# Performance work log

Hardware: AMD Instinct MI355X
Metric: run time of the kernel (lower is better)

## Reference

```python
import jax, jax.numpy as jnp
import numpy as np

ARCH = (1024, 2048, 2048, 512)
STEPS = 20
LR = 0.1
BATCH = 4096


def setup_inputs() -> dict:
    key = jax.random.key(0)
    ks = jax.random.split(key, 1 + len(ARCH) - 1)
    x = jax.random.normal(ks[0], (BATCH, ARCH[0]), dtype=jnp.float32)
    inp = {"x": x}
    # forward layers: weight (out, in) as in torch nn.Linear, orthogonal-ish init gain sqrt(2)
    for i in range(len(ARCH) - 1):
        fan_in = ARCH[i]
        W = jax.random.normal(ks[1 + i], (ARCH[i + 1], fan_in), dtype=jnp.float32) * jnp.sqrt(2.0 / fan_in)
        inp[f"W{i}"] = W
        inp[f"b{i}"] = jnp.zeros((ARCH[i + 1],), dtype=jnp.float32)
    return inp


def _errors(r, Ws):
    # errors[-1] = r[-1]; errors[i] = r[i] - tanh(F.linear(r[i+1], W_i.T)) = r[i] - tanh(r[i+1] @ W_i)
    errs = [None] * len(ARCH)
    errs[-1] = r[-1]
    for i in range(len(Ws) - 1, -1, -1):
        errs[i] = r[i] - jnp.tanh(r[i + 1] @ Ws[i])  # (B, arch[i])
    return errs


def _pc_forward(x, Ws, bs):
    # initialize states with a no-grad feedforward pass (torch.no_grad -> stop_gradient)
    r = [x]
    t = x
    for W, b in zip(Ws, bs):
        t = jnp.tanh(t @ W.T + b)
        r.append(jax.lax.stop_gradient(t))

    def step(carry, _):
        r = list(carry)
        errs = _errors(r, Ws)
        new_r = [r[0]]  # r[0] = x, fixed
        for i in range(1, len(ARCH)):
            feedback = errs[i - 1] @ Ws[i - 1].T  # F.linear(errors[i-1], W)
            new_r.append(r[i] + LR * (-errs[i] + feedback))
        return tuple(new_r), None

    r, _ = jax.lax.scan(step, tuple(r), None, length=STEPS)
    r = list(r)
    final_errs = _errors(r, Ws)
    total_error = 0.5 * sum(jnp.sum(e * e) for e in final_errs)
    return r[-1], total_error


def reference(x, W0, b0, W1, b1, W2, b2):
    Ws = [W0, W1, W2]
    bs = [b0, b1, b2]
    return _pc_forward(x, Ws, bs)
```

## Files before the change

### kernel.cpp

```cpp
#include <hip/hip_runtime.h>

typedef unsigned short u16;
typedef __bf16 bf16_t;
typedef bf16_t bf16x8 __attribute__((ext_vector_type(8)));
typedef u16 u16x8 __attribute__((ext_vector_type(8)));
typedef float f32x4 __attribute__((ext_vector_type(4)));

__device__ __forceinline__ u16 f2bf(float f) {
    unsigned u = __builtin_bit_cast(unsigned, f);
    u += 0x7fffu + ((u >> 16) & 1u);
    return (u16)(u >> 16);
}
__device__ __forceinline__ float bf2f(u16 h) {
    unsigned u = ((unsigned)h) << 16;
    return __builtin_bit_cast(float, u);
}
__device__ __forceinline__ float fast_tanh(float x) {
    x = fminf(fmaxf(x, -20.f), 20.f);
    float e = __expf(2.f * x);
    return (e - 1.f) * __builtin_amdgcn_rcpf(e + 1.f);
}
__device__ __forceinline__ void gload_lds16(const void* g, void* l) {
    __builtin_amdgcn_global_load_lds((__attribute__((address_space(1))) void*)(g),
                                     (__attribute__((address_space(3))) void*)(l),
                                     16, 0, 0);
}
__device__ __forceinline__ bf16x8 ld8(const u16* p) {
    return __builtin_bit_cast(bf16x8, *(const u16x8*)p);
}

#define VMW4() __builtin_amdgcn_s_waitcnt(0x3F74)
#define VMW0() __builtin_amdgcn_s_waitcnt(0x3F70)
#define MEMFENCE() asm volatile("" ::: "memory")
#define SCHED0() __builtin_amdgcn_sched_barrier(0)

#define GATE4() do { \
    MEMFENCE(); __builtin_amdgcn_s_barrier(); \
    asm volatile("s_waitcnt lgkmcnt(4)" ::: "memory"); \
    SCHED0(); \
} while (0)
#define LGKM0() do { \
    asm volatile("s_waitcnt lgkmcnt(0)" ::: "memory"); \
    SCHED0(); \
} while (0)
#define CLOSE() do { \
    SCHED0(); \
    MEMFENCE(); __builtin_amdgcn_s_barrier(); MEMFENCE(); \
} while (0)



__global__ void cvt_bf16(const float* __restrict__ src, u16* __restrict__ dst, int n4) {
    int i = blockIdx.x * blockDim.x + threadIdx.x;
    if (i < n4) {
        float4 v = ((const float4*)src)[i];
        ushort4 o;
        o.x = f2bf(v.x); o.y = f2bf(v.y); o.z = f2bf(v.z); o.w = f2bf(v.w);
        ((ushort4*)dst)[i] = o;
    }
}

__global__ void transpose_cvt(const float* __restrict__ W, u16* __restrict__ WT, int R, int C) {
    __shared__ float tile[32][33];
    int c0 = blockIdx.x * 32, r0 = blockIdx.y * 32;
    int tx = threadIdx.x & 31, ty = threadIdx.x >> 5;
#pragma unroll
    for (int i = 0; i < 32; i += 8)
        tile[ty + i][tx] = W[(size_t)(r0 + ty + i) * C + (c0 + tx)];
    __syncthreads();
#pragma unroll
    for (int i = 0; i < 32; i += 8)
        WT[(size_t)(c0 + ty + i) * R + (r0 + tx)] = f2bf(tile[tx][ty + i]);
}

__global__ void blockify(const u16* __restrict__ src, u16* __restrict__ dst, int K) {
    const int nk = K >> 5;
    const int rb = blockIdx.x / nk, cb = blockIdx.x % nk;
    const int t = threadIdx.x;
    const int kloc = (t & 7) * 4;
    u16* d = dst + (size_t)blockIdx.x * 4096 + ((kloc >> 3) << 10) + (kloc & 7);
    const u16* s = src + (size_t)(rb * 128) * K + cb * 32 + kloc;
#pragma unroll
    for (int p = 0; p < 4; ++p) {
        int row = (t >> 3) + p * 32;
        *(ushort4*)(d + row * 8) = *(const ushort4*)(s + (size_t)row * K);
    }
}


struct Seg {
    const u16* A; const u16* B;
    const u16* rsrcb;
    const float* rsrcf;
    const float* bias;
    const u16* esub;
    float* outf;
    u16* outbf;
    int K, N, blkStart, mode, accum;
};
struct Phase {
    Seg seg[3];
    int bEnd0, bEnd1;
};

#define ISSUE_A(dst, kk, mh) do { \
    const u16* _p = SH + buf * 16384 + (wr2 + (kk)) * 4096 + aoff + (mh) * 512; \
    dst[0] = ld8(_p); dst[1] = ld8(_p + 128); dst[2] = ld8(_p + 256); dst[3] = ld8(_p + 384); \
} while (0)

#define ISSUE_B(dst, kk) do { \
    const u16* _p = SH + 32768 + buf * 16384 + (wch2 + (kk)) * 4096 + boff; \
    dst[0] = ld8(_p); dst[1] = ld8(_p + 128); dst[2] = ld8(_p + 256); dst[3] = ld8(_p + 384); \
} while (0)

#define MFMACL(mh, A_, B_) do { \
    __builtin_amdgcn_s_setprio(1); \
    _Pragma("unroll") \
    for (int _i = 0; _i < 4; ++_i) { \
        _Pragma("unroll") \
        for (int _n = 0; _n < 4; ++_n) \
            acc[(mh) * 4 + _i][_n] = __builtin_amdgcn_mfma_f32_16x16x32_bf16( \
                A_[_i], B_[_n], acc[(mh) * 4 + _i][_n], 0, 0, 0); \
    } \
    __builtin_amdgcn_s_setprio(0); \
} while (0)

__global__ __launch_bounds__(512, 2) void pc_phase(Phase ph, float* __restrict__ errAcc) {
    __shared__ __align__(16) u16 SH[65536];
    __shared__ float red[8];

    const int bid = blockIdx.x;
    const int segi = (bid >= ph.bEnd0 ? 1 : 0) + (bid >= ph.bEnd1 ? 1 : 0);

    const u16* Ab = ph.seg[segi].A;
    const u16* Bb = ph.seg[segi].B;
    const int K = ph.seg[segi].K;
    const int local = bid - ph.seg[segi].blkStart;
    const int bx2 = local >> 4;
    const int by2 = local & 15;
    const int nk32 = K >> 5, NT = K >> 6;

    const int tid  = threadIdx.x;
    const int wave = tid >> 6, lane = tid & 63;
    const int q    = lane >> 4, ln = lane & 15;
    const int wr = wave >> 2, wc = wave & 3;
    const int wr2 = wr * 2, wch2 = (wc >> 1) * 2;
    const int aoff = q * 1024 + ln * 8;
    const int boff = q * 1024 + ((wc & 1) * 64 + ln) * 8;

    const size_t t8 = (size_t)tid * 8;
    const u16* gA0 = Ab + ((size_t)(by2 * 2 + 0) * nk32) * 4096 + t8;
    const u16* gA1 = Ab + ((size_t)(by2 * 2 + 1) * nk32) * 4096 + t8;
    const u16* gB0 = Bb + ((size_t)(bx2 * 2 + 0) * nk32) * 4096 + t8;
    const u16* gB1 = Bb + ((size_t)(bx2 * 2 + 1) * nk32) * 4096 + t8;
    const int wb = wave * 512;

    auto stageA = [&](int cb, int bf, int ks) {
        const size_t g = (size_t)cb * 4096;
        u16* a = SH + bf * 16384 + ks * 4096 + wb;
        gload_lds16(gA0 + g, a);
        gload_lds16(gA1 + g, a + 8192);
    };
    auto stageB = [&](int cb, int bf, int ks) {
        const size_t g = (size_t)cb * 4096;
        u16* b = SH + 32768 + bf * 16384 + ks * 4096 + wb;
        gload_lds16(gB0 + g, b);
        gload_lds16(gB1 + g, b + 8192);
    };

    f32x4 acc[8][4];
#pragma unroll
    for (int i = 0; i < 8; ++i)
#pragma unroll
        for (int j = 0; j < 4; ++j)
            acc[i][j] = (f32x4){0.f, 0.f, 0.f, 0.f};

    stageA(0, 0, 0); stageB(0, 0, 0);
    stageA(1, 0, 1); stageB(1, 0, 1);
    VMW4();
    MEMFENCE(); __builtin_amdgcn_s_barrier(); MEMFENCE();

    bf16x8 aRe[4], aRo[4], bR[4];

    for (int t = 0; t < NT; ++t) {
        const int buf = t & 1, nbuf = buf ^ 1;
        const int more = (t + 1 < NT);

        ISSUE_B(bR, 0); ISSUE_A(aRe, 0, 0); ISSUE_A(aRo, 0, 1);
        if (more) { stageA(2 * t + 2, nbuf, 0); stageB(2 * t + 2, nbuf, 0); }
        GATE4();
        MFMACL(0, aRe, bR);
        LGKM0();
        MFMACL(1, aRo, bR);
        if (more) VMW4(); else VMW0();
        CLOSE();

        ISSUE_B(bR, 1); ISSUE_A(aRe, 1, 0); ISSUE_A(aRo, 1, 1);
        if (more) { stageA(2 * t + 3, nbuf, 1); stageB(2 * t + 3, nbuf, 1); }
        GATE4();
        MFMACL(0, aRe, bR);
        LGKM0();
        MFMACL(1, aRo, bR);
        if (more) VMW4();
        CLOSE();
    }
    __syncthreads();

    const int N = ph.seg[segi].N;
    const int mode = ph.seg[segi].mode;
    const int accum = ph.seg[segi].accum;
    const u16* rsrcbP = ph.seg[segi].rsrcb;
    const float* rsrcfP = ph.seg[segi].rsrcf;
    const float* biasP = ph.seg[segi].bias;
    const u16* esubP = ph.seg[segi].esub;
    float* outfP = ph.seg[segi].outf;
    u16* outbfP = ph.seg[segi].outbf;

    const int nb32 = N >> 5;
    const size_t regOff = ((size_t)(by2 * 2 + wr) * nb32 + (size_t)(bx2 * 2 + (wc >> 1)) * 4) * 4096;
    u16* SLICE = SH + wave * 8192;

    float lsum = 0.f;
    const int rowg0 = by2 * 256 + wr * 128 + q * 4;
    const int colg0 = bx2 * 256 + wc * 64;

#pragma unroll
    for (int ct = 0; ct < 2; ++ct) {
        const size_t tileOff = regOff + (size_t)((wc & 1) * 2 + ct) * 4096;
        if (mode == 1 || mode == 2) {
#pragma unroll
            for (int p = 0; p < 8; ++p)
                *(u16x8*)(SLICE + p * 512 + lane * 8) =
                    *(const u16x8*)(rsrcbP + tileOff + p * 512 + lane * 8);
        }
        if (mode == 2) {
#pragma unroll
            for (int p = 0; p < 8; ++p)
                *(u16x8*)(SLICE + 4096 + p * 512 + lane * 8) =
                    *(const u16x8*)(esubP + tileOff + p * 512 + lane * 8);
        }
#pragma unroll
        for (int nh = 0; nh < 2; ++nh) {
            const int nt = ct * 2 + nh;
            const int ci = nh * 16 + ln;
            const int co = ((ci >> 3) & 3) * 1024 + (ci & 7);
            const int colg = colg0 + nt * 16 + ln;
            const float bnt = (mode == 0) ? biasP[colg] : 0.f;
#pragma unroll
            for (int mt = 0; mt < 8; ++mt) {
#pragma unroll
                for (int r = 0; r < 4; ++r) {
                    const int row = mt * 16 + q * 4 + r;
                    const int o = co + row * 8;
                    const float c = acc[mt][nt][r];
                    float v;
                    if (mode == 0) {
                        v = fast_tanh(c + bnt);
                        if (outfP) outfP[(size_t)(rowg0 + mt * 16 + r) * N + colg] = v;
                    } else if (mode == 1) {
                        v = bf2f(SLICE[o]) - fast_tanh(c);
                        if (accum) lsum += v * v;
                    } else if (mode == 2) {
                        v = bf2f(SLICE[o]) + 0.1f * (c - bf2f(SLICE[4096 + o]));
                    } else {
                        const size_t idx = (size_t)(rowg0 + mt * 16 + r) * N + colg;
                        v = 0.9f * rsrcfP[idx] + 0.1f * c;
                        outfP[idx] = v;
                        if (accum) lsum += v * v;
                    }
                    SLICE[o] = f2bf(v);
                }
            }
        }
#pragma unroll
        for (int p = 0; p < 8; ++p)
            *(u16x8*)(outbfP + tileOff + p * 512 + lane * 8) =
                *(const u16x8*)(SLICE + p * 512 + lane * 8);
    }

    if (accum) {
        lsum *= 0.5f;
#pragma unroll
        for (int o = 32; o > 0; o >>= 1) lsum += __shfl_down(lsum, o);
        if (lane == 0) red[wave] = lsum;
        __syncthreads();
        if (tid == 0) {
            float s = 0.f;
#pragma unroll
            for (int i = 0; i < 8; ++i) s += red[i];
            atomicAdd(errAcc, s);
        }
    }
}


extern "C" void kernel_launch(void* const* d_in, const int* in_sizes, int n_in,
                              void* d_out, int out_size, void* d_ws, size_t ws_size,
                              hipStream_t stream) {
    const float* x  = (const float*)d_in[0];
    const float* W0 = (const float*)d_in[1];
    const float* b0 = (const float*)d_in[2];
    const float* W1 = (const float*)d_in[3];
    const float* b1 = (const float*)d_in[4];
    const float* W2 = (const float*)d_in[5];
    const float* b2 = (const float*)d_in[6];

    const int Bz = 4096;

    char* ws = (char*)d_ws;
    size_t off = 0;
    auto alloc = [&](size_t bytes) -> char* {
        char* p = ws + off;
        off += (bytes + 255) & ~(size_t)255;
        return p;
    };

    u16*   r1b = (u16*)  alloc((size_t)Bz * 2048 * 2);
    u16*   r2b = (u16*)  alloc((size_t)Bz * 2048 * 2);
    u16*   r3b = (u16*)  alloc((size_t)Bz * 512 * 2);
    u16*   e0b = (u16*)  alloc((size_t)Bz * 1024 * 2);
    u16*   e1b = (u16*)  alloc((size_t)Bz * 2048 * 2);
    u16*   e2b = (u16*)  alloc((size_t)Bz * 2048 * 2);
    u16*   xb  = (u16*)  alloc((size_t)Bz * 1024 * 2);
    u16*   W0b = (u16*)  alloc((size_t)2048 * 1024 * 2);
    u16*   W0t = (u16*)  alloc((size_t)1024 * 2048 * 2);
    u16*   W1b = (u16*)  alloc((size_t)2048 * 2048 * 2);
    u16*   W1t = (u16*)  alloc((size_t)2048 * 2048 * 2);
    u16*   W2b = (u16*)  alloc((size_t)512 * 2048 * 2);
    u16*   W2t = (u16*)  alloc((size_t)2048 * 512 * 2);
    u16*   tmp = (u16*)  alloc((size_t)2048 * 2048 * 2);

    float* r3f    = (float*)d_out;
    float* errAcc = ((float*)d_out) + (size_t)Bz * 512;

    auto blkify = [&](const u16* s, u16* d, int M, int K) {
        blockify<<<(M / 128) * (K / 32), 256, 0, stream>>>(s, d, K);
    };

    cvt_bf16<<<(Bz * 1024 / 4) / 256, 256, 0, stream>>>(x, tmp, Bz * 1024 / 4);
    blkify(tmp, xb, Bz, 1024);
    cvt_bf16<<<(2048 * 1024 / 4) / 256, 256, 0, stream>>>(W0, tmp, 2048 * 1024 / 4);
    blkify(tmp, W0b, 2048, 1024);
    cvt_bf16<<<(2048 * 2048 / 4) / 256, 256, 0, stream>>>(W1, tmp, 2048 * 2048 / 4);
    blkify(tmp, W1b, 2048, 2048);
    cvt_bf16<<<(512 * 2048 / 4) / 256, 256, 0, stream>>>(W2, tmp, 512 * 2048 / 4);
    blkify(tmp, W2b, 512, 2048);
    transpose_cvt<<<dim3(1024 / 32, 2048 / 32), 256, 0, stream>>>(W0, tmp, 2048, 1024);
    blkify(tmp, W0t, 1024, 2048);
    transpose_cvt<<<dim3(2048 / 32, 2048 / 32), 256, 0, stream>>>(W1, tmp, 2048, 2048);
    blkify(tmp, W1t, 2048, 2048);
    transpose_cvt<<<dim3(2048 / 32, 512 / 32),  256, 0, stream>>>(W2, tmp, 512, 2048);
    blkify(tmp, W2t, 2048, 512);

    hipMemsetAsync(errAcc, 0, 4, stream);

    auto mkseg = [&](const u16* A, const u16* B, int K, int N,
                     const u16* rsrcb, const float* rsrcf, const float* bias,
                     const u16* esub, float* outf, u16* outbf,
                     int mode, int accum) {
        Seg s;
        s.A = A; s.B = B; s.rsrcb = rsrcb; s.rsrcf = rsrcf; s.bias = bias;
        s.esub = esub; s.outf = outf; s.outbf = outbf;
        s.K = K; s.N = N; s.blkStart = 0; s.mode = mode; s.accum = accum;
        return s;
    };
    auto nblk = [&](int N) { return (N / 256) * (Bz / 256); };

    auto launch1 = [&](Seg s0) {
        Phase ph;
        int b0c = nblk(s0.N);
        ph.seg[0] = s0; ph.seg[1] = s0; ph.seg[2] = s0;
        ph.bEnd0 = b0c; ph.bEnd1 = b0c;
        pc_phase<<<b0c, 512, 0, stream>>>(ph, errAcc);
    };
    auto launch3 = [&](Seg s0, Seg s1, Seg s2) {
        Phase ph;
        int b0c = nblk(s0.N), b1c = nblk(s1.N), b2c = nblk(s2.N);
        s1.blkStart = b0c; s2.blkStart = b0c + b1c;
        ph.seg[0] = s0; ph.seg[1] = s1; ph.seg[2] = s2;
        ph.bEnd0 = b0c; ph.bEnd1 = b0c + b1c;
        pc_phase<<<b0c + b1c + b2c, 512, 0, stream>>>(ph, errAcc);
    };

    launch1(mkseg(xb,  W0b, 1024, 2048, nullptr, nullptr, b0, nullptr, nullptr, r1b, 0, 0));
    launch1(mkseg(r1b, W1b, 2048, 2048, nullptr, nullptr, b1, nullptr, nullptr, r2b, 0, 0));
    launch1(mkseg(r2b, W2b, 2048, 512,  nullptr, nullptr, b2, nullptr, r3f,     r3b, 0, 0));

    for (int s = 0; s < 20; ++s) {
        int last = (s == 19) ? 1 : 0;
        launch3(mkseg(r2b, W1t, 2048, 2048, r1b, nullptr, nullptr, nullptr, nullptr, e1b, 1, 0),
                mkseg(r1b, W0t, 2048, 1024, xb,  nullptr, nullptr, nullptr, nullptr, e0b, 1, 0),
                mkseg(r3b, W2t, 512,  2048, r2b, nullptr, nullptr, nullptr, nullptr, e2b, 1, 0));
        launch3(mkseg(e1b, W1b, 2048, 2048, r2b, nullptr, nullptr, e2b, nullptr, r2b, 2, 0),
                mkseg(e2b, W2b, 2048, 512,  nullptr, r3f, nullptr, nullptr, r3f,  r3b, 3, last),
                mkseg(e0b, W0b, 1024, 2048, r1b, nullptr, nullptr, e1b, nullptr, r1b, 2, 0));
    }

    launch3(mkseg(r2b, W1t, 2048, 2048, r1b, nullptr, nullptr, nullptr, nullptr, e1b, 1, 1),
            mkseg(r1b, W0t, 2048, 1024, xb,  nullptr, nullptr, nullptr, nullptr, e0b, 1, 1),
            mkseg(r3b, W2t, 512,  2048, r2b, nullptr, nullptr, nullptr, nullptr, e2b, 1, 1));
}
```

Measured before the change: 3.662 ms.

## Let short-K segments process multiple output tiles per block to rebalance phases

Adds a per-segment tiles-per-block count, and each block loops over several output tiles, each with its own GEMM mainloop and epilogue. The short-K segments in the fused error and update phases are assigned two tiles per block, shrinking the grid. This aims to balance work against the long-K segments and reduce the number of co-resident blocks competing for CUs. In exchange it serializes work within those blocks and adds an extra barrier per tile.

```diff
diff --git a/kernel.cpp b/kernel.cpp
--- a/kernel.cpp
+++ b/kernel.cpp
@@ -97,6 +97,7 @@
     float* outf;
     u16* outbf;
     int K, N, blkStart, mode, accum;
+    int ntile, tpb;
 };
 struct Phase {
     Seg seg[3];
@@ -135,10 +136,10 @@
     const u16* Ab = ph.seg[segi].A;
     const u16* Bb = ph.seg[segi].B;
     const int K = ph.seg[segi].K;
-    const int local = bid - ph.seg[segi].blkStart;
-    const int bx2 = local >> 4;
-    const int by2 = local & 15;
     const int nk32 = K >> 5, NT = K >> 6;
+    const int tpb = ph.seg[segi].tpb;
+    const int ntile = ph.seg[segi].ntile;
+    const int lb = bid - ph.seg[segi].blkStart;
 
     const int tid  = threadIdx.x;
     const int wave = tid >> 6, lane = tid & 63;
@@ -147,64 +148,8 @@
     const int wr2 = wr * 2, wch2 = (wc >> 1) * 2;
     const int aoff = q * 1024 + ln * 8;
     const int boff = q * 1024 + ((wc & 1) * 64 + ln) * 8;
-
     const size_t t8 = (size_t)tid * 8;
-    const u16* gA0 = Ab + ((size_t)(by2 * 2 + 0) * nk32) * 4096 + t8;
-    const u16* gA1 = Ab + ((size_t)(by2 * 2 + 1) * nk32) * 4096 + t8;
-    const u16* gB0 = Bb + ((size_t)(bx2 * 2 + 0) * nk32) * 4096 + t8;
-    const u16* gB1 = Bb + ((size_t)(bx2 * 2 + 1) * nk32) * 4096 + t8;
     const int wb = wave * 512;
-
-    auto stageA = [&](int cb, int bf, int ks) {
-        const size_t g = (size_t)cb * 4096;
-        u16* a = SH + bf * 16384 + ks * 4096 + wb;
-        gload_lds16(gA0 + g, a);
-        gload_lds16(gA1 + g, a + 8192);
-    };
-    auto stageB = [&](int cb, int bf, int ks) {
-        const size_t g = (size_t)cb * 4096;
-        u16* b = SH + 32768 + bf * 16384 + ks * 4096 + wb;
-        gload_lds16(gB0 + g, b);
-        gload_lds16(gB1 + g, b + 8192);
-    };
-
-    f32x4 acc[8][4];
-#pragma unroll
-    for (int i = 0; i < 8; ++i)
-#pragma unroll
-        for (int j = 0; j < 4; ++j)
-            acc[i][j] = (f32x4){0.f, 0.f, 0.f, 0.f};
-
-    stageA(0, 0, 0); stageB(0, 0, 0);
-    stageA(1, 0, 1); stageB(1, 0, 1);
-    VMW4();
-    MEMFENCE(); __builtin_amdgcn_s_barrier(); MEMFENCE();
-
-    bf16x8 aRe[4], aRo[4], bR[4];
-
-    for (int t = 0; t < NT; ++t) {
-        const int buf = t & 1, nbuf = buf ^ 1;
-        const int more = (t + 1 < NT);
-
-        ISSUE_B(bR, 0); ISSUE_A(aRe, 0, 0); ISSUE_A(aRo, 0, 1);
-        if (more) { stageA(2 * t + 2, nbuf, 0); stageB(2 * t + 2, nbuf, 0); }
-        GATE4();
-        MFMACL(0, aRe, bR);
-        LGKM0();
-        MFMACL(1, aRo, bR);
-        if (more) VMW4(); else VMW0();
-        CLOSE();
-
-        ISSUE_B(bR, 1); ISSUE_A(aRe, 1, 0); ISSUE_A(aRo, 1, 1);
-        if (more) { stageA(2 * t + 3, nbuf, 1); stageB(2 * t + 3, nbuf, 1); }
-        GATE4();
-        MFMACL(0, aRe, bR);
-        LGKM0();
-        MFMACL(1, aRo, bR);
-        if (more) VMW4();
-        CLOSE();
-    }
-    __syncthreads();
 
     const int N = ph.seg[segi].N;
     const int mode = ph.seg[segi].mode;
@@ -215,80 +160,145 @@
     const u16* esubP = ph.seg[segi].esub;
     float* outfP = ph.seg[segi].outf;
     u16* outbfP = ph.seg[segi].outbf;
-
     const int nb32 = N >> 5;
-    const size_t regOff = ((size_t)(by2 * 2 + wr) * nb32 + (size_t)(bx2 * 2 + (wc >> 1)) * 4) * 4096;
-    u16* SLICE = SH + wave * 8192;
-
-    float lsum = 0.f;
-    const int rowg0 = by2 * 256 + wr * 128 + q * 4;
-    const int colg0 = bx2 * 256 + wc * 64;
-
-#pragma unroll
-    for (int ct = 0; ct < 2; ++ct) {
-        const size_t tileOff = regOff + (size_t)((wc & 1) * 2 + ct) * 4096;
-        if (mode == 1 || mode == 2) {
-#pragma unroll
-            for (int p = 0; p < 8; ++p)
-                *(u16x8*)(SLICE + p * 512 + lane * 8) =
-                    *(const u16x8*)(rsrcbP + tileOff + p * 512 + lane * 8);
+
+    for (int ti = 0; ti < tpb; ++ti) {
+        const int tileIdx = lb * tpb + ti;
+        if (tileIdx >= ntile) break;
+        const int bx2 = tileIdx >> 4;
+        const int by2 = tileIdx & 15;
+
+        const u16* gA0 = Ab + ((size_t)(by2 * 2 + 0) * nk32) * 4096 + t8;
+        const u16* gA1 = Ab + ((size_t)(by2 * 2 + 1) * nk32) * 4096 + t8;
+        const u16* gB0 = Bb + ((size_t)(bx2 * 2 + 0) * nk32) * 4096 + t8;
+        const u16* gB1 = Bb + ((size_t)(bx2 * 2 + 1) * nk32) * 4096 + t8;
+
+        auto stageA = [&](int cb, int bf, int ks) {
+            const size_t g = (size_t)cb * 4096;
+            u16* a = SH + bf * 16384 + ks * 4096 + wb;
+            gload_lds16(gA0 + g, a);
+            gload_lds16(gA1 + g, a + 8192);
+        };
+        auto stageB = [&](int cb, int bf, int ks) {
+            const size_t g = (size_t)cb * 4096;
+            u16* b = SH + 32768 + bf * 16384 + ks * 4096 + wb;
+            gload_lds16(gB0 + g, b);
+            gload_lds16(gB1 + g, b + 8192);
+        };
+
+        __syncthreads();
+
+        f32x4 acc[8][4];
+#pragma unroll
+        for (int i = 0; i < 8; ++i)
+#pragma unroll
+            for (int j = 0; j < 4; ++j)
+                acc[i][j] = (f32x4){0.f, 0.f, 0.f, 0.f};
+
+        stageA(0, 0, 0); stageB(0, 0, 0);
+        stageA(1, 0, 1); stageB(1, 0, 1);
+        VMW4();
+        MEMFENCE(); __builtin_amdgcn_s_barrier(); MEMFENCE();
+
+        bf16x8 aRe[4], aRo[4], bR[4];
+
+        for (int t = 0; t < NT; ++t) {
+            const int buf = t & 1, nbuf = buf ^ 1;
+            const int more = (t + 1 < NT);
+
+            ISSUE_B(bR, 0); ISSUE_A(aRe, 0, 0); ISSUE_A(aRo, 0, 1);
+            if (more) { stageA(2 * t + 2, nbuf, 0); stageB(2 * t + 2, nbuf, 0); }
+            GATE4();
+            MFMACL(0, aRe, bR);
+            LGKM0();
+            MFMACL(1, aRo, bR);
+            if (more) VMW4(); else VMW0();
+            CLOSE();
+
+            ISSUE_B(bR, 1); ISSUE_A(aRe, 1, 0); ISSUE_A(aRo, 1, 1);
+            if (more) { stageA(2 * t + 3, nbuf, 1); stageB(2 * t + 3, nbuf, 1); }
+            GATE4();
+            MFMACL(0, aRe, bR);
+            LGKM0();
+            MFMACL(1, aRo, bR);
+            if (more) VMW4();
+            CLOSE();
         }
-        if (mode == 2) {
-#pragma unroll
-            for (int p = 0; p < 8; ++p)
-                *(u16x8*)(SLICE + 4096 + p * 512 + lane * 8) =
-                    *(const u16x8*)(esubP + tileOff + p * 512 + lane * 8);
-        }
-#pragma unroll
-        for (int nh = 0; nh < 2; ++nh) {
-            const int nt = ct * 2 + nh;
-            const int ci = nh * 16 + ln;
-            const int co = ((ci >> 3) & 3) * 1024 + (ci & 7);
-            const int colg = colg0 + nt * 16 + ln;
-            const float bnt = (mode == 0) ? biasP[colg] : 0.f;
-#pragma unroll
-            for (int mt = 0; mt < 8; ++mt) {
-#pragma unroll
-                for (int r = 0; r < 4; ++r) {
-                    const int row = mt * 16 + q * 4 + r;
-                    const int o = co + row * 8;
-                    const float c = acc[mt][nt][r];
-                    float v;
-                    if (mode == 0) {
-                        v = fast_tanh(c + bnt);
-                        if (outfP) outfP[(size_t)(rowg0 + mt * 16 + r) * N + colg] = v;
-                    } else if (mode == 1) {
-                        v = bf2f(SLICE[o]) - fast_tanh(c);
-                        if (accum) lsum += v * v;
-                    } else if (mode == 2) {
-                        v = bf2f(SLICE[o]) + 0.1f * (c - bf2f(SLICE[4096 + o]));
-                    } else {
-                        const size_t idx = (size_t)(rowg0 + mt * 16 + r) * N + colg;
-                        v = 0.9f * rsrcfP[idx] + 0.1f * c;
-                        outfP[idx] = v;
-                        if (accum) lsum += v * v;
+        __syncthreads();
+
+        const size_t regOff = ((size_t)(by2 * 2 + wr) * nb32 + (size_t)(bx2 * 2 + (wc >> 1)) * 4) * 4096;
+        u16* SLICE = SH + wave * 8192;
+
+        float lsum = 0.f;
+        const int rowg0 = by2 * 256 + wr * 128 + q * 4;
+        const int colg0 = bx2 * 256 + wc * 64;
+
+#pragma unroll
+        for (int ct = 0; ct < 2; ++ct) {
+            const size_t tileOff = regOff + (size_t)((wc & 1) * 2 + ct) * 4096;
+            if (mode == 1 || mode == 2) {
+#pragma unroll
+                for (int p = 0; p < 8; ++p)
+                    *(u16x8*)(SLICE + p * 512 + lane * 8) =
+                        *(const u16x8*)(rsrcbP + tileOff + p * 512 + lane * 8);
+            }
+            if (mode == 2) {
+#pragma unroll
+                for (int p = 0; p < 8; ++p)
+                    *(u16x8*)(SLICE + 4096 + p * 512 + lane * 8) =
+                        *(const u16x8*)(esubP + tileOff + p * 512 + lane * 8);
+            }
+#pragma unroll
+            for (int nh = 0; nh < 2; ++nh) {
+                const int nt = ct * 2 + nh;
+                const int ci = nh * 16 + ln;
+                const int co = ((ci >> 3) & 3) * 1024 + (ci & 7);
+                const int colg = colg0 + nt * 16 + ln;
+                const float bnt = (mode == 0) ? biasP[colg] : 0.f;
+#pragma unroll
+                for (int mt = 0; mt < 8; ++mt) {
+#pragma unroll
+                    for (int r = 0; r < 4; ++r) {
+                        const int row = mt * 16 + q * 4 + r;
+                        const int o = co + row * 8;
+                        const float c = acc[mt][nt][r];
+                        float v;
+                        if (mode == 0) {
+                            v = fast_tanh(c + bnt);
+                            if (outfP) outfP[(size_t)(rowg0 + mt * 16 + r) * N + colg] = v;
+                        } else if (mode == 1) {
+                            v = bf2f(SLICE[o]) - fast_tanh(c);
+                            if (accum) lsum += v * v;
+                        } else if (mode == 2) {
+                            v = bf2f(SLICE[o]) + 0.1f * (c - bf2f(SLICE[4096 + o]));
+                        } else {
+                            const size_t idx = (size_t)(rowg0 + mt * 16 + r) * N + colg;
+                            v = 0.9f * rsrcfP[idx] + 0.1f * c;
+                            outfP[idx] = v;
+                            if (accum) lsum += v * v;
+                        }
+                        SLICE[o] = f2bf(v);
                     }
-                    SLICE[o] = f2bf(v);
                 }
             }
+#pragma unroll
+            for (int p = 0; p < 8; ++p)
+                *(u16x8*)(outbfP + tileOff + p * 512 + lane * 8) =
+                    *(const u16x8*)(SLICE + p * 512 + lane * 8);
         }
-#pragma unroll
-        for (int p = 0; p < 8; ++p)
-            *(u16x8*)(outbfP + tileOff + p * 512 + lane * 8) =
-                *(const u16x8*)(SLICE + p * 512 + lane * 8);
-    }
-
-    if (accum) {
-        lsum *= 0.5f;
-#pragma unroll
-        for (int o = 32; o > 0; o >>= 1) lsum += __shfl_down(lsum, o);
-        if (lane == 0) red[wave] = lsum;
-        __syncthreads();
-        if (tid == 0) {
-            float s = 0.f;
-#pragma unroll
-            for (int i = 0; i < 8; ++i) s += red[i];
-            atomicAdd(errAcc, s);
+
+        if (accum) {
+            lsum *= 0.5f;
+#pragma unroll
+            for (int o = 32; o > 0; o >>= 1) lsum += __shfl_down(lsum, o);
+            if (lane == 0) red[wave] = lsum;
+            __syncthreads();
+            if (tid == 0) {
+                float s = 0.f;
+#pragma unroll
+                for (int i = 0; i < 8; ++i) s += red[i];
+                atomicAdd(errAcc, s);
+            }
         }
     }
 }
@@ -362,21 +372,28 @@
         s.A = A; s.B = B; s.rsrcb = rsrcb; s.rsrcf = rsrcf; s.bias = bias;
         s.esub = esub; s.outf = outf; s.outbf = outbf;
         s.K = K; s.N = N; s.blkStart = 0; s.mode = mode; s.accum = accum;
+        s.ntile = 0; s.tpb = 1;
         return s;
     };
     auto nblk = [&](int N) { return (N / 256) * (Bz / 256); };
 
     auto launch1 = [&](Seg s0) {
         Phase ph;
-        int b0c = nblk(s0.N);
+        s0.ntile = nblk(s0.N); s0.tpb = 1; s0.blkStart = 0;
+        int b0c = s0.ntile;
         ph.seg[0] = s0; ph.seg[1] = s0; ph.seg[2] = s0;
         ph.bEnd0 = b0c; ph.bEnd1 = b0c;
         pc_phase<<<b0c, 512, 0, stream>>>(ph, errAcc);
     };
-    auto launch3 = [&](Seg s0, Seg s1, Seg s2) {
+    auto launch3 = [&](Seg s0, int t0, Seg s1, int t1, Seg s2, int t2) {
         Phase ph;
-        int b0c = nblk(s0.N), b1c = nblk(s1.N), b2c = nblk(s2.N);
-        s1.blkStart = b0c; s2.blkStart = b0c + b1c;
+        s0.ntile = nblk(s0.N); s0.tpb = t0;
+        s1.ntile = nblk(s1.N); s1.tpb = t1;
+        s2.ntile = nblk(s2.N); s2.tpb = t2;
+        int b0c = (s0.ntile + t0 - 1) / t0;
+        int b1c = (s1.ntile + t1 - 1) / t1;
+        int b2c = (s2.ntile + t2 - 1) / t2;
+        s0.blkStart = 0; s1.blkStart = b0c; s2.blkStart = b0c + b1c;
         ph.seg[0] = s0; ph.seg[1] = s1; ph.seg[2] = s2;
         ph.bEnd0 = b0c; ph.bEnd1 = b0c + b1c;
         pc_phase<<<b0c + b1c + b2c, 512, 0, stream>>>(ph, errAcc);
@@ -388,15 +405,15 @@
 
     for (int s = 0; s < 20; ++s) {
         int last = (s == 19) ? 1 : 0;
-        launch3(mkseg(r2b, W1t, 2048, 2048, r1b, nullptr, nullptr, nullptr, nullptr, e1b, 1, 0),
-                mkseg(r1b, W0t, 2048, 1024, xb,  nullptr, nullptr, nullptr, nullptr, e0b, 1, 0),
-                mkseg(r3b, W2t, 512,  2048, r2b, nullptr, nullptr, nullptr, nullptr, e2b, 1, 0));
-        launch3(mkseg(e1b, W1b, 2048, 2048, r2b, nullptr, nullptr, e2b, nullptr, r2b, 2, 0),
-                mkseg(e2b, W2b, 2048, 512,  nullptr, r3f, nullptr, nullptr, r3f,  r3b, 3, last),
-                mkseg(e0b, W0b, 1024, 2048, r1b, nullptr, nullptr, e1b, nullptr, r1b, 2, 0));
+        launch3(mkseg(r2b, W1t, 2048, 2048, r1b, nullptr, nullptr, nullptr, nullptr, e1b, 1, 0), 1,
+                mkseg(r1b, W0t, 2048, 1024, xb,  nullptr, nullptr, nullptr, nullptr, e0b, 1, 0), 1,
+                mkseg(r3b, W2t, 512,  2048, r2b, nullptr, nullptr, nullptr, nullptr, e2b, 1, 0), 2);
+        launch3(mkseg(e1b, W1b, 2048, 2048, r2b, nullptr, nullptr, e2b, nullptr, r2b, 2, 0), 1,
+                mkseg(e2b, W2b, 2048, 512,  nullptr, r3f, nullptr, nullptr, r3f,  r3b, 3, last), 1,
+                mkseg(e0b, W0b, 1024, 2048, r1b, nullptr, nullptr, e1b, nullptr, r1b, 2, 0), 2);
     }
 
-    launch3(mkseg(r2b, W1t, 2048, 2048, r1b, nullptr, nullptr, nullptr, nullptr, e1b, 1, 1),
-            mkseg(r1b, W0t, 2048, 1024, xb,  nullptr, nullptr, nullptr, nullptr, e0b, 1, 1),
-            mkseg(r3b, W2t, 512,  2048, r2b, nullptr, nullptr, nullptr, nullptr, e2b, 1, 1));
-}
+    launch3(mkseg(r2b, W1t, 2048, 2048, r1b, nullptr, nullptr, nullptr, nullptr, e1b, 1, 1), 1,
+            mkseg(r1b, W0t, 2048, 1024, xb,  nullptr, nullptr, nullptr, nullptr, e0b, 1, 1), 1,
+            mkseg(r3b, W2t, 512,  2048, r2b, nullptr, nullptr, nullptr, nullptr, e2b, 1, 1), 2);
+}
```

After: 3.769 ms. +2.9%, slower.

## Swizzle block-to-tile mapping, fuse f32 convert with blockify, skip unused final writes

Applied to the files above, without the earlier changes.

Changes the block-to-tile mapping so that groups of consecutive blocks cover a compact region of output tiles, improving L2 reuse of A and B panels across concurrently running blocks. Replaces the separate f32-to-bf16 conversion plus blockify passes for x and the forward weights with a single fused kernel, removing an intermediate buffer round trip. In the final error pass the bf16 error tiles are no longer written back, since only the accumulated error sum is needed. The new mapping assumes the block counts divide evenly into the chosen groups.

```diff
diff --git a/kernel.cpp b/kernel.cpp
--- a/kernel.cpp
+++ b/kernel.cpp
@@ -50,13 +50,20 @@
 
 
 
-__global__ void cvt_bf16(const float* __restrict__ src, u16* __restrict__ dst, int n4) {
-    int i = blockIdx.x * blockDim.x + threadIdx.x;
-    if (i < n4) {
-        float4 v = ((const float4*)src)[i];
+__global__ void blockify_f32(const float* __restrict__ src, u16* __restrict__ dst, int K) {
+    const int nk = K >> 5;
+    const int rb = blockIdx.x / nk, cb = blockIdx.x % nk;
+    const int t = threadIdx.x;
+    const int kloc = (t & 7) * 4;
+    u16* d = dst + (size_t)blockIdx.x * 4096 + ((kloc >> 3) << 10) + (kloc & 7);
+    const float* s = src + (size_t)(rb * 128) * K + cb * 32 + kloc;
+#pragma unroll
+    for (int p = 0; p < 4; ++p) {
+        int row = (t >> 3) + p * 32;
+        float4 v = *(const float4*)(s + (size_t)row * K);
         ushort4 o;
         o.x = f2bf(v.x); o.y = f2bf(v.y); o.z = f2bf(v.z); o.w = f2bf(v.w);
-        ((ushort4*)dst)[i] = o;
+        *(ushort4*)(d + row * 8) = o;
     }
 }
 
@@ -135,10 +142,17 @@
     const u16* Ab = ph.seg[segi].A;
     const u16* Bb = ph.seg[segi].B;
     const int K = ph.seg[segi].K;
+    const int N = ph.seg[segi].N;
     const int local = bid - ph.seg[segi].blkStart;
-    const int bx2 = local >> 4;
-    const int by2 = local & 15;
     const int nk32 = K >> 5, NT = K >> 6;
+
+    const int nbx = N >> 8;
+    const int bxc = nbx >> 1;
+    const int c = local & 7, sl = local >> 3;
+    const int sbx = (bxc > 0) ? (sl % (bxc ? bxc : 1)) : 0;
+    const int sby = (bxc > 0) ? (sl / (bxc ? bxc : 1)) : sl;
+    const int bx2 = (c & 1) * bxc + sbx;
+    const int by2 = (c >> 1) * 4 + sby;
 
     const int tid  = threadIdx.x;
     const int wave = tid >> 6, lane = tid & 63;
@@ -206,7 +220,6 @@
     }
     __syncthreads();
 
-    const int N = ph.seg[segi].N;
     const int mode = ph.seg[segi].mode;
     const int accum = ph.seg[segi].accum;
     const u16* rsrcbP = ph.seg[segi].rsrcb;
@@ -252,19 +265,19 @@
                 for (int r = 0; r < 4; ++r) {
                     const int row = mt * 16 + q * 4 + r;
                     const int o = co + row * 8;
-                    const float c = acc[mt][nt][r];
+                    const float c2 = acc[mt][nt][r];
                     float v;
                     if (mode == 0) {
-                        v = fast_tanh(c + bnt);
+                        v = fast_tanh(c2 + bnt);
                         if (outfP) outfP[(size_t)(rowg0 + mt * 16 + r) * N + colg] = v;
                     } else if (mode == 1) {
-                        v = bf2f(SLICE[o]) - fast_tanh(c);
+                        v = bf2f(SLICE[o]) - fast_tanh(c2);
                         if (accum) lsum += v * v;
                     } else if (mode == 2) {
-                        v = bf2f(SLICE[o]) + 0.1f * (c - bf2f(SLICE[4096 + o]));
+                        v = bf2f(SLICE[o]) + 0.1f * (c2 - bf2f(SLICE[4096 + o]));
                     } else {
                         const size_t idx = (size_t)(rowg0 + mt * 16 + r) * N + colg;
-                        v = 0.9f * rsrcfP[idx] + 0.1f * c;
+                        v = 0.9f * rsrcfP[idx] + 0.1f * c2;
                         outfP[idx] = v;
                         if (accum) lsum += v * v;
                     }
@@ -272,10 +285,12 @@
                 }
             }
         }
-#pragma unroll
-        for (int p = 0; p < 8; ++p)
-            *(u16x8*)(outbfP + tileOff + p * 512 + lane * 8) =
-                *(const u16x8*)(SLICE + p * 512 + lane * 8);
+        if (outbfP) {
+#pragma unroll
+            for (int p = 0; p < 8; ++p)
+                *(u16x8*)(outbfP + tileOff + p * 512 + lane * 8) =
+                    *(const u16x8*)(SLICE + p * 512 + lane * 8);
+        }
     }
 
     if (accum) {
@@ -336,15 +351,14 @@
     auto blkify = [&](const u16* s, u16* d, int M, int K) {
         blockify<<<(M / 128) * (K / 32), 256, 0, stream>>>(s, d, K);
     };
-
-    cvt_bf16<<<(Bz * 1024 / 4) / 256, 256, 0, stream>>>(x, tmp, Bz * 1024 / 4);
-    blkify(tmp, xb, Bz, 1024);
-    cvt_bf16<<<(2048 * 1024 / 4) / 256, 256, 0, stream>>>(W0, tmp, 2048 * 1024 / 4);
-    blkify(tmp, W0b, 2048, 1024);
-    cvt_bf16<<<(2048 * 2048 / 4) / 256, 256, 0, stream>>>(W1, tmp, 2048 * 2048 / 4);
-    blkify(tmp, W1b, 2048, 2048);
-    cvt_bf16<<<(512 * 2048 / 4) / 256, 256, 0, stream>>>(W2, tmp, 512 * 2048 / 4);
-    blkify(tmp, W2b, 512, 2048);
+    auto blkifyF = [&](const float* s, u16* d, int M, int K) {
+        blockify_f32<<<(M / 128) * (K / 32), 256, 0, stream>>>(s, d, K);
+    };
+
+    blkifyF(x,  xb,  Bz,   1024);
+    blkifyF(W0, W0b, 2048, 1024);
+    blkifyF(W1, W1b, 2048, 2048);
+    blkifyF(W2, W2b, 512,  2048);
     transpose_cvt<<<dim3(1024 / 32, 2048 / 32), 256, 0, stream>>>(W0, tmp, 2048, 1024);
     blkify(tmp, W0t, 1024, 2048);
     transpose_cvt<<<dim3(2048 / 32, 2048 / 32), 256, 0, stream>>>(W1, tmp, 2048, 2048);
@@ -396,7 +410,7 @@
                 mkseg(e0b, W0b, 1024, 2048, r1b, nullptr, nullptr, e1b, nullptr, r1b, 2, 0));
     }
 
-    launch3(mkseg(r2b, W1t, 2048, 2048, r1b, nullptr, nullptr, nullptr, nullptr, e1b, 1, 1),
-            mkseg(r1b, W0t, 2048, 1024, xb,  nullptr, nullptr, nullptr, nullptr, e0b, 1, 1),
-            mkseg(r3b, W2t, 512,  2048, r2b, nullptr, nullptr, nullptr, nullptr, e2b, 1, 1));
-}
+    launch3(mkseg(r2b, W1t, 2048, 2048, r1b, nullptr, nullptr, nullptr, nullptr, nullptr, 1, 1),
+            mkseg(r1b, W0t, 2048, 1024, xb,  nullptr, nullptr, nullptr, nullptr, nullptr, 1, 1),
+            mkseg(r3b, W2t, 512,  2048, r2b, nullptr, nullptr, nullptr, nullptr, nullptr, 1, 1));
+}
```

Result: no change. 3.676 ms (+0.4%).
